# Optimization experiments

Measured on AMD Instinct MI355X. Metric: run time of the kernel, lower is better.

The kernel has to match this reference:

```python
import jax, jax.numpy as jnp
import numpy as np


def _derive_cayley():
    basis_gens = [(), (1,), (2,), (3,), (1, 2), (1, 3), (2, 3), (1, 2, 3)]
    gens_to_idx = {g: i for i, g in enumerate(basis_gens)}

    def reduce(a, b):
        gens = list(a) + list(b)
        sign = 1
        changed = True
        while changed:
            changed = False
            i = 0
            while i < len(gens) - 1:
                if gens[i] == gens[i + 1]:
                    gens.pop(i); gens.pop(i)
                    changed = True
                    if i > 0:
                        i -= 1
                elif gens[i] > gens[i + 1]:
                    gens[i], gens[i + 1] = gens[i + 1], gens[i]
                    sign *= -1
                    changed = True
                    i += 1
                else:
                    i += 1
        return gens_to_idx[tuple(gens)], sign

    K = np.zeros((8, 8), dtype=np.int32)   # target blade of product i*j
    S = np.zeros((8, 8), dtype=np.float32)  # sign of product i*j
    for i in range(8):
        for j in range(8):
            k, s = reduce(basis_gens[i], basis_gens[j])
            K[i, j] = k
            S[i, j] = s
    return K, S

_K, _S = _derive_cayley()
_I, _J = np.meshgrid(np.arange(8), np.arange(8), indexing='ij')
_K_FLAT = jnp.asarray(_K.reshape(-1))
_I_FLAT = jnp.asarray(_I.reshape(-1))
_J_FLAT = jnp.asarray(_J.reshape(-1))
_S_FLAT = jnp.asarray(_S.reshape(-1))

LN_EPS = 1e-5


def setup_inputs() -> dict:
    key = jax.random.key(0)
    ks = jax.random.split(key, 4)
    N_tok, D, F = 4096, 1024, 4096
    x = jax.random.normal(ks[0], (N_tok, 8, D), dtype=jnp.float32)
    interaction_weights = jnp.ones((64,), dtype=jnp.float32) * 0.1
    geo_gate = jnp.asarray(0.5, dtype=jnp.float32)
    ln_w = jnp.ones((D,), dtype=jnp.float32)
    ln_b = jnp.zeros((D,), dtype=jnp.float32)
    s = 0.02
    w_gate = jax.random.normal(ks[1], (D, F), dtype=jnp.float32) * s
    w_up = jax.random.normal(ks[2], (D, F), dtype=jnp.float32) * s
    w_down = jax.random.normal(ks[3], (F, D), dtype=jnp.float32) * s
    return {"x": x, "interaction_weights": interaction_weights, "geo_gate": geo_gate,
            "ln_w": ln_w, "ln_b": ln_b, "w_gate": w_gate, "w_up": w_up, "w_down": w_down}


def reference(x, interaction_weights, geo_gate, ln_w, ln_b, w_gate, w_up, w_down):
    dtype = x.dtype
    # sparse bilinear coefficient tensor C[k, i, j] = sign(i,j) * sigmoid(w)[i*8+j]
    w = jax.nn.sigmoid(interaction_weights).astype(dtype)  # (64,)
    C = jnp.zeros((8, 8, 8), dtype=dtype).at[_K_FLAT, _I_FLAT, _J_FLAT].set(_S_FLAT.astype(dtype) * w)
    # geometric product: geo[n,k,d] = sum_ij C[k,i,j] x[n,i,d] x[n,j,d]
    geo = jnp.einsum('kij,nid,njd->nkd', C, x, x)
    g = jax.nn.sigmoid(geo_gate).astype(dtype)
    mixed = g * geo + (1.0 - g) * x  # (N, 8, D)
    # LayerNorm over last dim D
    mu = jnp.mean(mixed, axis=-1, keepdims=True)
    var = jnp.mean(jnp.square(mixed - mu), axis=-1, keepdims=True)
    flat = (mixed - mu) * jax.lax.rsqrt(var + LN_EPS) * ln_w + ln_b
    # SwiGLU MLP
    h = jax.nn.silu(flat @ w_gate) * (flat @ w_up)  # (N, 8, F)
    out = h @ w_down  # (N, 8, D)
    return x + out
```

## Files before the change

kernel.cpp:

```cpp
#include <hip/hip_runtime.h>

typedef unsigned short u16;
using bf16x8 = __attribute__((ext_vector_type(8))) __bf16;
using f32x4  = __attribute__((ext_vector_type(4))) float;
using u16x4  = __attribute__((ext_vector_type(4))) unsigned short;

#define D_DIM 1024
#define F_DIM 4096

struct Cayley { int k[8][8]; int s[8][8]; };
constexpr Cayley make_cayley() {
    Cayley c{};
    const int gens[8][3] = {{0,0,0},{1,0,0},{2,0,0},{3,0,0},{1,2,0},{1,3,0},{2,3,0},{1,2,3}};
    const int glen[8] = {0,1,1,1,2,2,2,3};
    const int mask2idx[8] = {0,1,2,4,3,5,6,7};
    for (int i = 0; i < 8; ++i) {
        for (int j = 0; j < 8; ++j) {
            int g[6] = {0,0,0,0,0,0};
            int n = 0;
            for (int t = 0; t < glen[i]; ++t) g[n++] = gens[i][t];
            for (int t = 0; t < glen[j]; ++t) g[n++] = gens[j][t];
            int sign = 1;
            bool changed = true;
            while (changed) {
                changed = false;
                int t = 0;
                while (t + 1 < n) {
                    if (g[t] == g[t+1]) {
                        for (int u = t; u + 2 < n; ++u) g[u] = g[u+2];
                        n -= 2; changed = true;
                        if (t > 0) --t;
                    } else if (g[t] > g[t+1]) {
                        int tmp = g[t]; g[t] = g[t+1]; g[t+1] = tmp;
                        sign = -sign; changed = true; ++t;
                    } else {
                        ++t;
                    }
                }
            }
            int mask = 0;
            for (int t = 0; t < n; ++t) mask |= 1 << (g[t] - 1);
            c.k[i][j] = mask2idx[mask];
            c.s[i][j] = sign;
        }
    }
    return c;
}
constexpr Cayley CAY = make_cayley();

__device__ __forceinline__ u16 f2bf(float f) {
    unsigned u = __float_as_uint(f);
    unsigned r = 0x7FFFu + ((u >> 16) & 1u);
    return (u16)((u + r) >> 16);
}

__device__ __forceinline__ void gload16(const u16* g, const u16* l) {
    __builtin_amdgcn_global_load_lds(
        (const __attribute__((address_space(1))) void*)g,
        (__attribute__((address_space(3))) void*)l, 16, 0, 0);
}

__device__ __forceinline__ bf16x8 frag(const u16* tile, int row, int ks, int lane) {
    const int slot = ((ks << 2) + (lane >> 4)) ^ (lane & 7);
    return *(const bf16x8*)(tile + row * 64 + slot * 8);
}

__global__ __launch_bounds__(256) void transpose_kernel(
    const float* __restrict__ in, u16* __restrict__ outp, int R, int C, int mode)
{
    __shared__ float tile[32][33];
    const int tx = threadIdx.x & 31, ty = threadIdx.x >> 5;
    const int c0 = blockIdx.x * 32, r0 = blockIdx.y * 32;
    #pragma unroll
    for (int t = 0; t < 4; ++t)
        tile[ty + t*8][tx] = in[(size_t)(r0 + ty + t*8) * C + c0 + tx];
    __syncthreads();
    #pragma unroll
    for (int t = 0; t < 4; ++t) {
        const int c = c0 + ty + t*8;
        int orow;
        if (mode == 0)      orow = c;
        else if (mode == 1) orow = ((c >> 4) << 5) + (c & 15);
        else                orow = ((c >> 4) << 5) + 16 + (c & 15);
        outp[(size_t)orow * R + r0 + tx] = f2bf(tile[tx][ty + t*8]);
    }
}

__global__ __launch_bounds__(256, 2) void geo_ln_kernel(
    const float* __restrict__ x, const float* __restrict__ iw,
    const float* __restrict__ gg, const float* __restrict__ lnw,
    const float* __restrict__ lnb, u16* __restrict__ flat)
{
    __shared__ float wsig[64];
    __shared__ float red[4][16];
    const int tid = threadIdx.x;
    if (tid < 64) wsig[tid] = 1.f / (1.f + __expf(-iw[tid]));
    __syncthreads();
    const float g   = 1.f / (1.f + __expf(-gg[0]));
    const float gm1 = 1.f - g;

    float coef[64];
    #pragma unroll
    for (int t = 0; t < 64; ++t) coef[t] = (float)CAY.s[t >> 3][t & 7] * wsig[t];

    const int n  = blockIdx.x;
    const int d0 = tid * 4;
    const float* xb = x + (size_t)n * 8 * D_DIM;
    f32x4 xv[8];
    #pragma unroll
    for (int i = 0; i < 8; ++i) xv[i] = __builtin_nontemporal_load((const f32x4*)(xb + i * D_DIM + d0));

    float mix[8][4];
    #pragma unroll
    for (int s4 = 0; s4 < 4; ++s4) {
        float xs[8];
        #pragma unroll
        for (int i = 0; i < 8; ++i) xs[i] = xv[i][s4];
        float geo[8] = {0.f,0.f,0.f,0.f,0.f,0.f,0.f,0.f};
        #pragma unroll
        for (int i = 0; i < 8; ++i) {
            #pragma unroll
            for (int j = 0; j < 8; ++j) {
                geo[CAY.k[i][j]] = fmaf(coef[i*8+j] * xs[i], xs[j], geo[CAY.k[i][j]]);
            }
        }
        #pragma unroll
        for (int k = 0; k < 8; ++k) mix[k][s4] = g * geo[k] + gm1 * xs[k];
    }

    float s1[8], s2[8];
    #pragma unroll
    for (int k = 0; k < 8; ++k) {
        s1[k] = 0.f; s2[k] = 0.f;
        #pragma unroll
        for (int s4 = 0; s4 < 4; ++s4) {
            s1[k] += mix[k][s4];
            s2[k]  = fmaf(mix[k][s4], mix[k][s4], s2[k]);
        }
    }
    #pragma unroll
    for (int m = 1; m < 64; m <<= 1) {
        #pragma unroll
        for (int k = 0; k < 8; ++k) {
            s1[k] += __shfl_xor(s1[k], m, 64);
            s2[k] += __shfl_xor(s2[k], m, 64);
        }
    }
    const int wave = tid >> 6, lane = tid & 63;
    if (lane == 0) {
        #pragma unroll
        for (int k = 0; k < 8; ++k) { red[wave][k] = s1[k]; red[wave][8+k] = s2[k]; }
    }
    __syncthreads();
    float mean[8], rstd[8];
    #pragma unroll
    for (int k = 0; k < 8; ++k) {
        float a = red[0][k] + red[1][k] + red[2][k] + red[3][k];
        float b = red[0][8+k] + red[1][8+k] + red[2][8+k] + red[3][8+k];
        float mu  = a * (1.f / 1024.f);
        float var = b * (1.f / 1024.f) - mu * mu;
        mean[k] = mu;
        rstd[k] = rsqrtf(var + 1e-5f);
    }
    f32x4 lw = *(const f32x4*)(lnw + d0);
    f32x4 lb = *(const f32x4*)(lnb + d0);
    #pragma unroll
    for (int k = 0; k < 8; ++k) {
        u16x4 o;
        #pragma unroll
        for (int s4 = 0; s4 < 4; ++s4) {
            float v = (mix[k][s4] - mean[k]) * rstd[k] * lw[s4] + lb[s4];
            o[s4] = f2bf(v);
        }
        *(u16x4*)(flat + ((size_t)(n * 8 + k)) * D_DIM + d0) = o;
    }
}

template<int KDIM, bool S1, bool S2, int W>
__device__ __forceinline__ void ktile2(
    int t, const u16* __restrict__ A, const u16* __restrict__ B,
    u16 (*As)[256][64], u16 (*Bs)[256][64],
    int brow, int bcol, int wave, int lane, int wm, int wn, int fr,
    f32x4 (&acc)[8][4])
{
    const int buf = t & 1;
    const int nbuf = (t + 1) & 1;
    const u16* At = &As[buf][0][0];
    const u16* Bt = &Bs[buf][0][0];
    const int sr = lane >> 3, sslot = (lane & 7) ^ sr;

    bf16x8 af[4][2], bf0[2][2], bf1[2][2];

    #pragma unroll
    for (int m = 0; m < 4; ++m)
        #pragma unroll
        for (int ks = 0; ks < 2; ++ks)
            af[m][ks] = frag(At, wm*64 + m*16 + fr, ks, lane);
    #pragma unroll
    for (int n = 0; n < 2; ++n)
        #pragma unroll
        for (int ks = 0; ks < 2; ++ks) {
            bf0[n][ks] = frag(Bt, wn*32 + n*16 + fr, ks, lane);
            bf1[n][ks] = frag(Bt, 128 + wn*32 + n*16 + fr, ks, lane);
        }
    if (S1) {
        #pragma unroll
        for (int q = 0; q < 2; ++q) {
            const int idx_w = q*512 + wave*64;
            const int row = (idx_w >> 3) + sr;
            gload16(A + (size_t)(brow + 128 + row)*KDIM + (t+1)*64 + sslot*8,
                    &As[nbuf][128][0] + idx_w*8);
        }
        #pragma unroll
        for (int q = 0; q < 2; ++q) {
            const int idx_w = q*512 + wave*64;
            const int row = (idx_w >> 3) + sr;
            gload16(B + (size_t)(bcol + 128 + row)*KDIM + (t+1)*64 + sslot*8,
                    &Bs[nbuf][128][0] + idx_w*8);
        }
    }
    __builtin_amdgcn_s_setprio(1);
    #pragma unroll
    for (int m = 0; m < 4; ++m)
        #pragma unroll
        for (int n = 0; n < 2; ++n)
            #pragma unroll
            for (int ks = 0; ks < 2; ++ks) {
                acc[m][n]   = __builtin_amdgcn_mfma_f32_16x16x32_bf16(af[m][ks], bf0[n][ks], acc[m][n],   0, 0, 0);
                acc[m][2+n] = __builtin_amdgcn_mfma_f32_16x16x32_bf16(af[m][ks], bf1[n][ks], acc[m][2+n], 0, 0, 0);
            }
    __builtin_amdgcn_s_setprio(0);
    __builtin_amdgcn_s_barrier();
    __builtin_amdgcn_sched_barrier(0);

    #pragma unroll
    for (int m = 0; m < 4; ++m)
        #pragma unroll
        for (int ks = 0; ks < 2; ++ks)
            af[m][ks] = frag(At, 128 + wm*64 + m*16 + fr, ks, lane);
    if (S2) {
        #pragma unroll
        for (int q = 0; q < 2; ++q) {
            const int idx_w = q*512 + wave*64;
            const int row = (idx_w >> 3) + sr;
            gload16(A + (size_t)(brow + row)*KDIM + (t+2)*64 + sslot*8,
                    &As[buf][0][0] + idx_w*8);
        }
        #pragma unroll
        for (int q = 0; q < 2; ++q) {
            const int idx_w = q*512 + wave*64;
            const int row = (idx_w >> 3) + sr;
            gload16(B + (size_t)(bcol + row)*KDIM + (t+2)*64 + sslot*8,
                    &Bs[buf][0][0] + idx_w*8);
        }
    }
    __builtin_amdgcn_s_setprio(1);
    #pragma unroll
    for (int m = 0; m < 4; ++m)
        #pragma unroll
        for (int n = 0; n < 2; ++n)
            #pragma unroll
            for (int ks = 0; ks < 2; ++ks) {
                acc[4+m][n]   = __builtin_amdgcn_mfma_f32_16x16x32_bf16(af[m][ks], bf0[n][ks], acc[4+m][n],   0, 0, 0);
                acc[4+m][2+n] = __builtin_amdgcn_mfma_f32_16x16x32_bf16(af[m][ks], bf1[n][ks], acc[4+m][2+n], 0, 0, 0);
            }
    __builtin_amdgcn_s_setprio(0);
    if constexpr (W == 4)      asm volatile("s_waitcnt vmcnt(4)" ::: "memory");
    else if constexpr (W == 0) asm volatile("s_waitcnt vmcnt(0)" ::: "memory");
    __builtin_amdgcn_s_barrier();
    __builtin_amdgcn_sched_barrier(0);
}

template<int KDIM, int EPI>
__global__ __launch_bounds__(512, 2) void gemm8ph(
    const u16* __restrict__ A, const u16* __restrict__ B,
    const float* __restrict__ X, void* __restrict__ OUT, int Ncols)
{
    constexpr int NT = KDIM / 64;
    __shared__ alignas(16) u16 As[2][256][64];
    __shared__ alignas(16) u16 Bs[2][256][64];

    const int nbx = Ncols >> 8;
    const int nwg = gridDim.x;
    const int bid = blockIdx.x;
    int brow, bcol;
    if constexpr (EPI == 1) {
        const int xcd = bid & 7, idx = bid >> 3;
        const int cpx = nbx >> 3;
        bcol = (xcd * cpx + (idx & (cpx - 1))) << 8;
        brow = (idx / cpx) << 8;
    } else {
        const int wg = (bid & 7) * (nwg >> 3) + (bid >> 3);
        brow = (wg / nbx) << 8;
        bcol = (wg % nbx) << 8;
    }

    const int tid = threadIdx.x;
    const int wave = tid >> 6, lane = tid & 63;
    const int wm = wave >> 2, wn = wave & 3;
    const int fr = lane & 15, fq = lane >> 4;
    const int sr = lane >> 3, sslot = (lane & 7) ^ sr;

    f32x4 acc[8][4];
    #pragma unroll
    for (int i = 0; i < 8; ++i)
        #pragma unroll
        for (int j = 0; j < 4; ++j) acc[i][j] = {0.f, 0.f, 0.f, 0.f};

    #pragma unroll
    for (int q = 0; q < 2; ++q) {
        const int idx_w = q*512 + wave*64;
        const int row = (idx_w >> 3) + sr;
        gload16(A + (size_t)(brow + row)*KDIM + sslot*8,          &As[0][0][0]   + idx_w*8);
    }
    #pragma unroll
    for (int q = 0; q < 2; ++q) {
        const int idx_w = q*512 + wave*64;
        const int row = (idx_w >> 3) + sr;
        gload16(B + (size_t)(bcol + row)*KDIM + sslot*8,          &Bs[0][0][0]   + idx_w*8);
    }
    #pragma unroll
    for (int q = 0; q < 2; ++q) {
        const int idx_w = q*512 + wave*64;
        const int row = (idx_w >> 3) + sr;
        gload16(A + (size_t)(brow + 128 + row)*KDIM + sslot*8,    &As[0][128][0] + idx_w*8);
    }
    #pragma unroll
    for (int q = 0; q < 2; ++q) {
        const int idx_w = q*512 + wave*64;
        const int row = (idx_w >> 3) + sr;
        gload16(B + (size_t)(bcol + 128 + row)*KDIM + sslot*8,    &Bs[0][128][0] + idx_w*8);
    }
    #pragma unroll
    for (int q = 0; q < 2; ++q) {
        const int idx_w = q*512 + wave*64;
        const int row = (idx_w >> 3) + sr;
        gload16(A + (size_t)(brow + row)*KDIM + 64 + sslot*8,     &As[1][0][0]   + idx_w*8);
    }
    #pragma unroll
    for (int q = 0; q < 2; ++q) {
        const int idx_w = q*512 + wave*64;
        const int row = (idx_w >> 3) + sr;
        gload16(B + (size_t)(bcol + row)*KDIM + 64 + sslot*8,     &Bs[1][0][0]   + idx_w*8);
    }
    asm volatile("s_waitcnt vmcnt(4)" ::: "memory");
    __builtin_amdgcn_s_barrier();
    __builtin_amdgcn_sched_barrier(0);

    #pragma unroll 1
    for (int t = 0; t < NT - 2; ++t)
        ktile2<KDIM, true, true, 4>(t, A, B, As, Bs, brow, bcol, wave, lane, wm, wn, fr, acc);
    ktile2<KDIM, true,  false, 0>(NT-2, A, B, As, Bs, brow, bcol, wave, lane, wm, wn, fr, acc);
    ktile2<KDIM, false, false, -1>(NT-1, A, B, As, Bs, brow, bcol, wave, lane, wm, wn, fr, acc);

    if constexpr (EPI == 1) {
        u16* H = (u16*)OUT;
        const int Nh = Ncols >> 1;
        #pragma unroll
        for (int qm = 0; qm < 2; ++qm)
            #pragma unroll
            for (int m = 0; m < 4; ++m) {
                const int row = brow + qm*128 + wm*64 + m*16 + fq*4;
                #pragma unroll
                for (int qn = 0; qn < 2; ++qn) {
                    const int col = (bcol >> 1) + qn*64 + wn*16 + fr;
                    f32x4 g = acc[qm*4+m][qn*2+0];
                    f32x4 u = acc[qm*4+m][qn*2+1];
                    #pragma unroll
                    for (int r = 0; r < 4; ++r) {
                        float gv = g[r], uv = u[r];
                        float hv = (gv / (1.f + __expf(-gv))) * uv;
                        __builtin_nontemporal_store(f2bf(hv), &H[(size_t)(row + r) * Nh + col]);
                    }
                }
            }
    } else {
        float* Of = (float*)OUT;
        #pragma unroll
        for (int mi = 0; mi < 8; ++mi) {
            const int row = brow + (mi>>2)*128 + wm*64 + (mi&3)*16 + fq*4;
            #pragma unroll
            for (int ni = 0; ni < 4; ++ni) {
                const int col = bcol + (ni>>1)*128 + wn*32 + (ni&1)*16 + fr;
                #pragma unroll
                for (int r = 0; r < 4; ++r) {
                    float xv = __builtin_nontemporal_load(&X[(size_t)(row+r)*Ncols + col]);
                    __builtin_nontemporal_store(xv + acc[mi][ni][r], &Of[(size_t)(row+r)*Ncols + col]);
                }
            }
        }
    }
}

extern "C" void kernel_launch(void* const* d_in, const int* in_sizes, int n_in,
                              void* d_out, int out_size, void* d_ws, size_t ws_size,
                              hipStream_t stream) {
    const float* x     = (const float*)d_in[0];
    const float* iw    = (const float*)d_in[1];
    const float* gg    = (const float*)d_in[2];
    const float* lnw   = (const float*)d_in[3];
    const float* lnb   = (const float*)d_in[4];
    const float* wgate = (const float*)d_in[5];
    const float* wup   = (const float*)d_in[6];
    const float* wdown = (const float*)d_in[7];
    float* out = (float*)d_out;

    const int ntok = in_sizes[0] / (8 * D_DIM);
    const int M    = ntok * 8;

    const size_t flat_b = (size_t)M * D_DIM * 2;
    const size_t wc_b   = (size_t)2 * D_DIM * F_DIM * 2;
    const size_t wd_b   = (size_t)D_DIM * F_DIM * 2;
    const size_t h_b    = (size_t)M * F_DIM * 2;
    const size_t need   = flat_b + wc_b + wd_b + h_b;
    if (ws_size < need) return;

    char* ws = (char*)d_ws;
    u16* flat = (u16*)(ws);
    u16* wc   = (u16*)(ws + flat_b);
    u16* wdt  = (u16*)(ws + flat_b + wc_b);
    u16* h    = (u16*)(ws + flat_b + wc_b + wd_b);

    transpose_kernel<<<dim3(F_DIM/32, D_DIM/32), 256, 0, stream>>>(wgate, wc,  D_DIM, F_DIM, 1);
    transpose_kernel<<<dim3(F_DIM/32, D_DIM/32), 256, 0, stream>>>(wup,   wc,  D_DIM, F_DIM, 2);
    transpose_kernel<<<dim3(D_DIM/32, F_DIM/32), 256, 0, stream>>>(wdown, wdt, F_DIM, D_DIM, 0);
    geo_ln_kernel<<<dim3(ntok), 256, 0, stream>>>(x, iw, gg, lnw, lnb, flat);

    gemm8ph<D_DIM, 1><<<dim3((M/256) * (2*F_DIM/256)), 512, 0, stream>>>(flat, wc, nullptr, h, 2*F_DIM);
    gemm8ph<F_DIM, 0><<<dim3((M/256) * (D_DIM/256)), 512, 0, stream>>>(h, wdt, x, out, D_DIM);
}
```

Before: 832.2 us.

## Restructure GEMM mainloop into eight-phase schedule with finer-grained staging

Replaces the two-phase-per-k-tile GEMM loop with an eight-phase loop covering two k-tiles per iteration. Each phase issues one quarter-tile global-to-LDS load, reads only the fragments it needs, and runs a 16-MFMA block between barriers, with explicit lgkmcnt/vmcnt waits. The aim is to spread memory traffic evenly across the compute and overlap LDS reads with MFMA more tightly, similar to the HipKittens 8-wave ping-pong schedule. The cost is many more barriers per k-tile and hand-tuned wait counts that are fragile to get right.

Result: slower. 945.8 us (+13.7%).

```diff
diff --git a/kernel.cpp b/kernel.cpp
--- a/kernel.cpp
+++ b/kernel.cpp
@@ -65,6 +65,52 @@
     return *(const bf16x8*)(tile + row * 64 + slot * 8);
 }
 
+__device__ __forceinline__ void stage_half(
+    const u16* __restrict__ G, int baseRow, int kt, u16* ldsHalf,
+    int wave, int sr, int sslot, int KD)
+{
+    #pragma unroll
+    for (int q = 0; q < 2; ++q) {
+        const int idx_w = q*512 + wave*64;
+        const int row = (idx_w >> 3) + sr;
+        gload16(G + (size_t)(baseRow + row)*KD + kt*64 + sslot*8, ldsHalf + idx_w*8);
+    }
+}
+
+__device__ __forceinline__ void rdA(bf16x8 (&af)[4][2], const u16* T, int base, int fr, int lane) {
+    #pragma unroll
+    for (int m = 0; m < 4; ++m)
+        #pragma unroll
+        for (int ks = 0; ks < 2; ++ks)
+            af[m][ks] = frag(T, base + m*16 + fr, ks, lane);
+}
+
+__device__ __forceinline__ void rdB(bf16x8 (&bf)[2][2], const u16* T, int base, int fr, int lane) {
+    #pragma unroll
+    for (int n = 0; n < 2; ++n)
+        #pragma unroll
+        for (int ks = 0; ks < 2; ++ks)
+            bf[n][ks] = frag(T, base + n*16 + fr, ks, lane);
+}
+
+__device__ __forceinline__ void mm16(f32x4 (&acc)[8][4], int mo, int no,
+                                     bf16x8 (&af)[4][2], bf16x8 (&bf)[2][2]) {
+    __builtin_amdgcn_s_setprio(1);
+    #pragma unroll
+    for (int m = 0; m < 4; ++m)
+        #pragma unroll
+        for (int n = 0; n < 2; ++n)
+            #pragma unroll
+            for (int ks = 0; ks < 2; ++ks)
+                acc[mo+m][no+n] = __builtin_amdgcn_mfma_f32_16x16x32_bf16(af[m][ks], bf[n][ks], acc[mo+m][no+n], 0, 0, 0);
+    __builtin_amdgcn_s_setprio(0);
+}
+
+#define BAR()  __builtin_amdgcn_s_barrier()
+#define SB0()  __builtin_amdgcn_sched_barrier(0)
+#define LG0()  do { asm volatile("s_waitcnt lgkmcnt(0)" ::: "memory"); SB0(); } while (0)
+#define VM(N)  asm volatile("s_waitcnt vmcnt(" #N ")" ::: "memory")
+
 __global__ __launch_bounds__(256) void transpose_kernel(
     const float* __restrict__ in, u16* __restrict__ outp, int R, int C, int mode)
 {
@@ -176,99 +222,73 @@
     }
 }
 
-template<int KDIM, bool S1, bool S2, int W>
-__device__ __forceinline__ void ktile2(
-    int t, const u16* __restrict__ A, const u16* __restrict__ B,
+template<int KDIM, bool LAST>
+__device__ __forceinline__ void iter8(
+    int i, const u16* __restrict__ A, const u16* __restrict__ B,
     u16 (*As)[256][64], u16 (*Bs)[256][64],
     int brow, int bcol, int wave, int lane, int wm, int wn, int fr,
     f32x4 (&acc)[8][4])
 {
-    const int buf = t & 1;
-    const int nbuf = (t + 1) & 1;
-    const u16* At = &As[buf][0][0];
-    const u16* Bt = &Bs[buf][0][0];
+    const int tb = 2*i + 1, na = 2*i + 2, nb = 2*i + 3;
+    const u16* At0 = &As[0][0][0];
+    const u16* Bt0 = &Bs[0][0][0];
+    const u16* At1 = &As[1][0][0];
+    const u16* Bt1 = &Bs[1][0][0];
     const int sr = lane >> 3, sslot = (lane & 7) ^ sr;
 
     bf16x8 af[4][2], bf0[2][2], bf1[2][2];
 
-    #pragma unroll
-    for (int m = 0; m < 4; ++m)
-        #pragma unroll
-        for (int ks = 0; ks < 2; ++ks)
-            af[m][ks] = frag(At, wm*64 + m*16 + fr, ks, lane);
-    #pragma unroll
-    for (int n = 0; n < 2; ++n)
-        #pragma unroll
-        for (int ks = 0; ks < 2; ++ks) {
-            bf0[n][ks] = frag(Bt, wn*32 + n*16 + fr, ks, lane);
-            bf1[n][ks] = frag(Bt, 128 + wn*32 + n*16 + fr, ks, lane);
-        }
-    if (S1) {
-        #pragma unroll
-        for (int q = 0; q < 2; ++q) {
-            const int idx_w = q*512 + wave*64;
-            const int row = (idx_w >> 3) + sr;
-            gload16(A + (size_t)(brow + 128 + row)*KDIM + (t+1)*64 + sslot*8,
-                    &As[nbuf][128][0] + idx_w*8);
-        }
-        #pragma unroll
-        for (int q = 0; q < 2; ++q) {
-            const int idx_w = q*512 + wave*64;
-            const int row = (idx_w >> 3) + sr;
-            gload16(B + (size_t)(bcol + 128 + row)*KDIM + (t+1)*64 + sslot*8,
-                    &Bs[nbuf][128][0] + idx_w*8);
-        }
-    }
-    __builtin_amdgcn_s_setprio(1);
-    #pragma unroll
-    for (int m = 0; m < 4; ++m)
-        #pragma unroll
-        for (int n = 0; n < 2; ++n)
-            #pragma unroll
-            for (int ks = 0; ks < 2; ++ks) {
-                acc[m][n]   = __builtin_amdgcn_mfma_f32_16x16x32_bf16(af[m][ks], bf0[n][ks], acc[m][n],   0, 0, 0);
-                acc[m][2+n] = __builtin_amdgcn_mfma_f32_16x16x32_bf16(af[m][ks], bf1[n][ks], acc[m][2+n], 0, 0, 0);
-            }
-    __builtin_amdgcn_s_setprio(0);
-    __builtin_amdgcn_s_barrier();
-    __builtin_amdgcn_sched_barrier(0);
-
-    #pragma unroll
-    for (int m = 0; m < 4; ++m)
-        #pragma unroll
-        for (int ks = 0; ks < 2; ++ks)
-            af[m][ks] = frag(At, 128 + wm*64 + m*16 + fr, ks, lane);
-    if (S2) {
-        #pragma unroll
-        for (int q = 0; q < 2; ++q) {
-            const int idx_w = q*512 + wave*64;
-            const int row = (idx_w >> 3) + sr;
-            gload16(A + (size_t)(brow + row)*KDIM + (t+2)*64 + sslot*8,
-                    &As[buf][0][0] + idx_w*8);
-        }
-        #pragma unroll
-        for (int q = 0; q < 2; ++q) {
-            const int idx_w = q*512 + wave*64;
-            const int row = (idx_w >> 3) + sr;
-            gload16(B + (size_t)(bcol + row)*KDIM + (t+2)*64 + sslot*8,
-                    &Bs[buf][0][0] + idx_w*8);
-        }
-    }
-    __builtin_amdgcn_s_setprio(1);
-    #pragma unroll
-    for (int m = 0; m < 4; ++m)
-        #pragma unroll
-        for (int n = 0; n < 2; ++n)
-            #pragma unroll
-            for (int ks = 0; ks < 2; ++ks) {
-                acc[4+m][n]   = __builtin_amdgcn_mfma_f32_16x16x32_bf16(af[m][ks], bf0[n][ks], acc[4+m][n],   0, 0, 0);
-                acc[4+m][2+n] = __builtin_amdgcn_mfma_f32_16x16x32_bf16(af[m][ks], bf1[n][ks], acc[4+m][2+n], 0, 0, 0);
-            }
-    __builtin_amdgcn_s_setprio(0);
-    if constexpr (W == 4)      asm volatile("s_waitcnt vmcnt(4)" ::: "memory");
-    else if constexpr (W == 0) asm volatile("s_waitcnt vmcnt(0)" ::: "memory");
-    __builtin_amdgcn_s_barrier();
-    __builtin_amdgcn_sched_barrier(0);
+    rdA(af, At0, wm*64, fr, lane);
+    rdB(bf0, Bt0, wn*32, fr, lane);
+    stage_half(A, brow+128, tb, &As[1][128][0], wave, sr, sslot, KDIM);
+    asm volatile("s_waitcnt lgkmcnt(8)" ::: "memory");
+    BAR(); LG0();
+    mm16(acc, 0, 0, af, bf0);
+    VM(6);
+    BAR(); SB0();
+
+    rdB(bf1, Bt0, 128 + wn*32, fr, lane);
+    stage_half(B, bcol+128, tb, &Bs[1][128][0], wave, sr, sslot, KDIM);
+    BAR(); LG0();
+    mm16(acc, 0, 2, af, bf1);
+    BAR(); SB0();
+
+    rdA(af, At0, 128 + wm*64, fr, lane);
+    if (!LAST) stage_half(A, brow, na, &As[0][0][0], wave, sr, sslot, KDIM);
+    BAR(); LG0();
+    mm16(acc, 4, 0, af, bf0);
+    BAR(); SB0();
+
+    if (!LAST) stage_half(B, bcol, na, &Bs[0][0][0], wave, sr, sslot, KDIM);
+    mm16(acc, 4, 2, af, bf1);
+    if (LAST) VM(4); else VM(8);
+    BAR(); SB0();
+
+    rdA(af, At1, wm*64, fr, lane);
+    rdB(bf0, Bt1, wn*32, fr, lane);
+    if (!LAST) stage_half(A, brow+128, na, &As[0][128][0], wave, sr, sslot, KDIM);
+    asm volatile("s_waitcnt lgkmcnt(8)" ::: "memory");
+    BAR(); LG0();
+    mm16(acc, 0, 0, af, bf0);
+    if (LAST) VM(0); else VM(6);
+    BAR(); SB0();
+
+    rdB(bf1, Bt1, 128 + wn*32, fr, lane);
+    if (!LAST) stage_half(B, bcol+128, na, &Bs[0][128][0], wave, sr, sslot, KDIM);
+    BAR(); LG0();
+    mm16(acc, 0, 2, af, bf1);
+    BAR(); SB0();
+
+    rdA(af, At1, 128 + wm*64, fr, lane);
+    if (!LAST) stage_half(A, brow, nb, &As[1][0][0], wave, sr, sslot, KDIM);
+    BAR(); LG0();
+    mm16(acc, 4, 0, af, bf0);
+    BAR(); SB0();
+
+    if (!LAST) stage_half(B, bcol, nb, &Bs[1][0][0], wave, sr, sslot, KDIM);
+    mm16(acc, 4, 2, af, bf1);
+    if (!LAST) VM(8);
+    BAR(); SB0();
 }
 
 template<int KDIM, int EPI>
@@ -277,6 +297,8 @@
     const float* __restrict__ X, void* __restrict__ OUT, int Ncols)
 {
     constexpr int NT = KDIM / 64;
+    constexpr int NI = NT / 2;
+    static_assert(NT % 2 == 0, "NT must be even");
     __shared__ alignas(16) u16 As[2][256][64];
     __shared__ alignas(16) u16 Bs[2][256][64];
 
@@ -307,51 +329,19 @@
         #pragma unroll
         for (int j = 0; j < 4; ++j) acc[i][j] = {0.f, 0.f, 0.f, 0.f};
 
-    #pragma unroll
-    for (int q = 0; q < 2; ++q) {
-        const int idx_w = q*512 + wave*64;
-        const int row = (idx_w >> 3) + sr;
-        gload16(A + (size_t)(brow + row)*KDIM + sslot*8,          &As[0][0][0]   + idx_w*8);
-    }
-    #pragma unroll
-    for (int q = 0; q < 2; ++q) {
-        const int idx_w = q*512 + wave*64;
-        const int row = (idx_w >> 3) + sr;
-        gload16(B + (size_t)(bcol + row)*KDIM + sslot*8,          &Bs[0][0][0]   + idx_w*8);
-    }
-    #pragma unroll
-    for (int q = 0; q < 2; ++q) {
-        const int idx_w = q*512 + wave*64;
-        const int row = (idx_w >> 3) + sr;
-        gload16(A + (size_t)(brow + 128 + row)*KDIM + sslot*8,    &As[0][128][0] + idx_w*8);
-    }
-    #pragma unroll
-    for (int q = 0; q < 2; ++q) {
-        const int idx_w = q*512 + wave*64;
-        const int row = (idx_w >> 3) + sr;
-        gload16(B + (size_t)(bcol + 128 + row)*KDIM + sslot*8,    &Bs[0][128][0] + idx_w*8);
-    }
-    #pragma unroll
-    for (int q = 0; q < 2; ++q) {
-        const int idx_w = q*512 + wave*64;
-        const int row = (idx_w >> 3) + sr;
-        gload16(A + (size_t)(brow + row)*KDIM + 64 + sslot*8,     &As[1][0][0]   + idx_w*8);
-    }
-    #pragma unroll
-    for (int q = 0; q < 2; ++q) {
-        const int idx_w = q*512 + wave*64;
-        const int row = (idx_w >> 3) + sr;
-        gload16(B + (size_t)(bcol + row)*KDIM + 64 + sslot*8,     &Bs[1][0][0]   + idx_w*8);
-    }
-    asm volatile("s_waitcnt vmcnt(4)" ::: "memory");
-    __builtin_amdgcn_s_barrier();
-    __builtin_amdgcn_sched_barrier(0);
+    stage_half(A, brow,     0, &As[0][0][0],   wave, sr, sslot, KDIM);
+    stage_half(B, bcol,     0, &Bs[0][0][0],   wave, sr, sslot, KDIM);
+    stage_half(A, brow+128, 0, &As[0][128][0], wave, sr, sslot, KDIM);
+    stage_half(B, bcol+128, 0, &Bs[0][128][0], wave, sr, sslot, KDIM);
+    stage_half(A, brow,     1, &As[1][0][0],   wave, sr, sslot, KDIM);
+    stage_half(B, bcol,     1, &Bs[1][0][0],   wave, sr, sslot, KDIM);
+    VM(8);
+    BAR(); SB0();
 
     #pragma unroll 1
-    for (int t = 0; t < NT - 2; ++t)
-        ktile2<KDIM, true, true, 4>(t, A, B, As, Bs, brow, bcol, wave, lane, wm, wn, fr, acc);
-    ktile2<KDIM, true,  false, 0>(NT-2, A, B, As, Bs, brow, bcol, wave, lane, wm, wn, fr, acc);
-    ktile2<KDIM, false, false, -1>(NT-1, A, B, As, Bs, brow, bcol, wave, lane, wm, wn, fr, acc);
+    for (int i = 0; i < NI - 1; ++i)
+        iter8<KDIM, false>(i, A, B, As, Bs, brow, bcol, wave, lane, wm, wn, fr, acc);
+    iter8<KDIM, true>(NI - 1, A, B, As, Bs, brow, bcol, wave, lane, wm, wn, fr, acc);
 
     if constexpr (EPI == 1) {
         u16* H = (u16*)OUT;
```
